# Performance work log

Hardware: AMD Instinct MI355X
Metric: run time of the kernel (lower is better)

The kernel has to match this reference:

```python
import jax, jax.numpy as jnp
import numpy as np

B, S = 2, 2048                 # batch, prefill seq len
H, HKV, D = 32, 8, 128          # num_heads, num_kv_heads, head_size
G = H // HKV                    # queries per kv head (GQA)
BLOCK_SIZE, NUM_BLOCKS = 128, 128
SCALE = 1.0 / (D ** 0.5)
NEG_INF = -1e9


def setup_inputs() -> dict:
    key = jax.random.key(0)
    kq, kk, kv, kc = jax.random.split(key, 4)
    query = jax.random.normal(kq, (B, S, H * D), dtype=jnp.float32)
    key_t = jax.random.normal(kk, (B, S, HKV * D), dtype=jnp.float32)
    value = jax.random.normal(kv, (B, S, HKV * D), dtype=jnp.float32)
    kv_cache = jax.random.normal(kc, (2, NUM_BLOCKS, BLOCK_SIZE, HKV, D), dtype=jnp.float32)
    tok = jnp.arange(B * S)
    block_indices = (tok // BLOCK_SIZE).astype(jnp.int32)   # in [0, NUM_BLOCKS)
    block_offsets = (tok % BLOCK_SIZE).astype(jnp.int32)    # in [0, BLOCK_SIZE)
    causal = jnp.tril(jnp.ones((S, S), dtype=bool))
    attn_bias = jnp.where(causal, 0.0, NEG_INF).astype(jnp.float32)[None, None]  # [1,1,S,S]
    return {"query": query, "key": key_t, "value": value, "kv_cache": kv_cache,
            "block_indices": block_indices, "block_offsets": block_offsets,
            "attn_bias": attn_bias}


def reference(query, key, value, kv_cache, block_indices, block_offsets, attn_bias):
    # --- KV cache scatter write (VLLMKVCache insert) ---
    k_tok = key.reshape(-1, HKV, D)     # [num_tokens, HKV, D]
    v_tok = value.reshape(-1, HKV, D)
    key_cache = kv_cache[0].at[block_indices, block_offsets].set(k_tok)
    value_cache = kv_cache[1].at[block_indices, block_offsets].set(v_tok)

    # --- prefill attention (xops.prompt_attention with GQA) ---
    q = query.reshape(B, S, HKV, G, D)            # split heads into kv groups
    kh = key.reshape(B, S, HKV, D)
    vh = value.reshape(B, S, HKV, D)
    scores = jnp.einsum('bqhgd,bkhd->bhgqk', q, kh) * SCALE  # [B,HKV,G,S,S]
    scores = scores + attn_bias[:, :, None]                   # bias broadcast over h,g
    probs = jax.nn.softmax(scores, axis=-1)
    out = jnp.einsum('bhgqk,bkhd->bqhgd', probs, vh)          # [B,S,HKV,G,D]
    output = out.reshape(B, S, H * D)
    return output, key_cache, value_cache
```

## Files before the change

kernel.cpp:

```cpp
#include <hip/hip_runtime.h>
#include <hip/hip_bf16.h>
#include <stdint.h>

#define B_ 2
#define S_ 2048
#define HKV_ 8
#define D_ 128

#define KVB 32
#define KTILE_SH 4096
#define VROWS 40
#define VTILE_SH 5120
#define LDSBUF 18432

typedef __attribute__((ext_vector_type(8))) short bf16x8;
typedef __attribute__((ext_vector_type(16))) float f32x16;
typedef __attribute__((ext_vector_type(4))) int int4v;

typedef const __attribute__((address_space(1))) void gv_t;
typedef __attribute__((address_space(3))) void lv_t;

__device__ __forceinline__ unsigned pk2(float lo, float hi) {
  unsigned r;
  asm("v_cvt_pk_bf16_f32 %0, %1, %2" : "=v"(r) : "v"(lo), "v"(hi));
  return r;
}
__device__ __forceinline__ void plswap(unsigned& a, unsigned& b) {
  asm volatile("v_permlane32_swap_b32 %0, %1" : "+v"(a), "+v"(b));
}
__device__ __forceinline__ bf16x8 frag4(unsigned a, unsigned b, unsigned c, unsigned d) {
  union { int4v i; bf16x8 v; } u;
  u.i = int4v{(int)a, (int)b, (int)c, (int)d};
  return u.v;
}


__global__ void cache_copy_kernel(const float4* __restrict__ src,
                                  float4* __restrict__ dst, int n4) {
  int i = blockIdx.x * blockDim.x + threadIdx.x;
  if (i < n4) dst[i] = src[i];
}


__global__ __launch_bounds__(256)
void prep_kernel(const float* __restrict__ K, const float* __restrict__ V,
                 const int* __restrict__ bi, const int* __restrict__ bo,
                 float* __restrict__ kc, float* __restrict__ vc,
                 short* __restrict__ kimg, short* __restrict__ vimg) {
  __shared__ float Vf[KVB * 132];
  const int bid = blockIdx.x;
  const int hg  = bid & 15;
  const int kt  = bid >> 4;
  const int kvh = hg & 7;
  const int b   = hg >> 3;
  const int tid = threadIdx.x;
  const int kv0 = kt * KVB;
  const float* kb = K + (int64_t)b * S_ * 1024 + kvh * 128;
  const float* vb = V + (int64_t)b * S_ * 1024 + kvh * 128;
  short* kimg_t = kimg + (int64_t)(hg * 64 + kt) * KTILE_SH;
  short* vimg_t = vimg + (int64_t)(hg * 64 + kt) * VTILE_SH;
#pragma unroll
  for (int i = 0; i < 4; ++i) {
    int idx = i * 256 + tid;
    int key = idx >> 5;
    int d0  = (idx & 31) * 4;
    int64_t roff = (int64_t)(kv0 + key) * 1024 + d0;
    float4 kf = *(const float4*)(kb + roff);
    float4 vf = *(const float4*)(vb + roff);
    int tok = b * S_ + kv0 + key;
    int64_t slot = (int64_t)bi[tok] * 128 + bo[tok];
    *(float4*)(kc + slot * 1024 + kvh * 128 + d0) = kf;
    *(float4*)(vc + slot * 1024 + kvh * 128 + d0) = vf;
    unsigned k01 = pk2(kf.x, kf.y), k23 = pk2(kf.z, kf.w);
    int koff = key * 128 + (d0 ^ ((key & 7) << 3));
    int2 st; st.x = (int)k01; st.y = (int)k23;
    *(int2*)(kimg_t + koff) = st;
    *(float4*)(&Vf[key * 132 + d0]) = vf;
  }
  __syncthreads();
  const int d  = tid & 127;
  const int kg = tid >> 7;
  const int k0 = kg * 16;
  unsigned uu[8];
#pragma unroll
  for (int i2 = 0; i2 < 8; ++i2)
    uu[i2] = pk2(Vf[(k0 + 2 * i2) * 132 + d], Vf[(k0 + 2 * i2 + 1) * 132 + d]);
  *(int4v*)(vimg_t + d * VROWS + k0)     = int4v{(int)uu[0], (int)uu[1], (int)uu[2], (int)uu[3]};
  *(int4v*)(vimg_t + d * VROWS + k0 + 8) = int4v{(int)uu[4], (int)uu[5], (int)uu[6], (int)uu[7]};
}


__global__ __launch_bounds__(256, 3)
void attn_kernel(const float* __restrict__ Q, const short* __restrict__ kimg,
                 const short* __restrict__ vimg, float* __restrict__ O) {
  __shared__ int4v ldsv[2 * LDSBUF / 16];
  char* ldsb = (char*)ldsv;

  const int bid = blockIdx.x;
  const int hg  = bid & 15;
  const int cc  = 63 - (bid >> 4);
  const int kvh = hg & 7;
  const int b   = hg >> 3;

  const int tid = threadIdx.x;
  const int w   = tid >> 6;
  const int l   = tid & 63;
  const int c31 = l & 31;
  const int hi  = l >> 5;
  const int qi  = c31 & 15;
  const int hh  = c31 >> 4;
  const int qoff = cc * 32 + (w & 1) * 16;
  const int qrow = qoff + qi;
  const int h    = kvh * 4 + (w >> 1) * 2 + hh;
  const int sw   = (c31 & 7) << 3;

  const float qscale = 0.08838834764831845f * 1.4426950408889634f;

  const float* qp = Q + ((int64_t)(b * S_ + qrow)) * 4096 + h * 128;
  bf16x8 qf[8];
#pragma unroll
  for (int ks = 0; ks < 8; ++ks) {
    int d0 = ks * 16 + hi * 8;
    float4 x = *(const float4*)(qp + d0);
    float4 y = *(const float4*)(qp + d0 + 4);
    qf[ks] = frag4(pk2(x.x * qscale, x.y * qscale), pk2(x.z * qscale, x.w * qscale),
                   pk2(y.x * qscale, y.y * qscale), pk2(y.z * qscale, y.w * qscale));
  }

  f32x16 acc[4];
#pragma unroll
  for (int dt = 0; dt < 4; ++dt)
#pragma unroll
    for (int r = 0; r < 16; ++r) acc[dt][r] = 0.f;
  float m = -1e30f, lsum = 0.f;

  const int nkt = cc + 1;
  const short* kimg_b = kimg + (int64_t)(hg * 64) * KTILE_SH;
  const short* vimg_b = vimg + (int64_t)(hg * 64) * VTILE_SH;

#define STAGE(KT, BUF)                                                          \
  do {                                                                          \
    const short* kg_ = kimg_b + (int64_t)(KT) * KTILE_SH;                       \
    const short* vg_ = vimg_b + (int64_t)(KT) * VTILE_SH;                       \
    char* kd_ = ldsb + (BUF) * LDSBUF;                                          \
    char* vd_ = kd_ + 8192;                                                     \
    _Pragma("unroll")                                                           \
    for (int i_ = 0; i_ < 2; ++i_) {                                            \
      int u_ = i_ * 256 + w * 64;                                               \
      __builtin_amdgcn_global_load_lds((gv_t*)(const void*)(kg_ + (u_ + l) * 8),\
                                       (lv_t*)(void*)(kd_ + u_ * 16), 16, 0, 0);\
    }                                                                           \
    _Pragma("unroll")                                                           \
    for (int i_ = 0; i_ < 3; ++i_) {                                            \
      int u_ = i_ * 256 + w * 64;                                               \
      if (u_ < 640) {                                                           \
        __builtin_amdgcn_global_load_lds((gv_t*)(const void*)(vg_ + (u_ + l) * 8),\
                                         (lv_t*)(void*)(vd_ + u_ * 16), 16, 0, 0);\
      }                                                                         \
    }                                                                           \
  } while (0)

  STAGE(0, 0);

  for (int kt = 0; kt < nkt; ++kt) {
    __syncthreads();
    const int cur = kt & 1;
    if (kt + 1 < nkt) STAGE(kt + 1, cur ^ 1);
    const short* kl = (const short*)(ldsb + cur * LDSBUF);
    const short* vl = (const short*)(ldsb + cur * LDSBUF + 8192);
    const int kv0 = kt * KVB;

    f32x16 s;
#pragma unroll
    for (int r = 0; r < 16; ++r) s[r] = 0.f;
#pragma unroll
    for (int ks = 0; ks < 8; ++ks) {
      int koff = c31 * 128 + ((ks * 16 + hi * 8) ^ sw);
      bf16x8 kf = *(const bf16x8*)(kl + koff);
      s = __builtin_amdgcn_mfma_f32_32x32x16_bf16(kf, qf[ks], s, 0, 0, 0);
    }

    if (kv0 + 31 > qoff) {
#pragma unroll
      for (int r = 0; r < 16; ++r) {
        int key = kv0 + (r & 3) + 8 * (r >> 2) + 4 * hi;
        if (key > qrow) s[r] = -1e30f;
      }
    }

    float qm = s[0];
#pragma unroll
    for (int r = 1; r < 16; ++r) qm = fmaxf(qm, s[r]);
    qm = fmaxf(qm, __shfl_xor(qm, 32));
    if (__any(qm > m + 11.0f)) {
      float mn = fmaxf(m, qm);
      float al = exp2f(m - mn);
      m = mn; lsum *= al;
#pragma unroll
      for (int dt = 0; dt < 4; ++dt)
#pragma unroll
        for (int r = 0; r < 16; ++r) acc[dt][r] *= al;
    }
    float su = 0.f;
#pragma unroll
    for (int r = 0; r < 16; ++r) {
      float p = exp2f(s[r] - m);
      s[r] = p;
      su += p;
    }
    lsum += su;

    unsigned u0 = pk2(s[0], s[1]),  u1 = pk2(s[2], s[3]);
    unsigned u2 = pk2(s[4], s[5]),  u3 = pk2(s[6], s[7]);
    unsigned u4 = pk2(s[8], s[9]),  u5 = pk2(s[10], s[11]);
    unsigned u6 = pk2(s[12], s[13]), u7 = pk2(s[14], s[15]);
    plswap(u0, u2); plswap(u1, u3);
    plswap(u4, u6); plswap(u5, u7);
    bf16x8 pf0 = frag4(u0, u1, u2, u3);
    bf16x8 pf1 = frag4(u4, u5, u6, u7);

#pragma unroll
    for (int ks2 = 0; ks2 < 2; ++ks2) {
      bf16x8 pf = ks2 ? pf1 : pf0;
#pragma unroll
      for (int dt = 0; dt < 4; ++dt) {
        const short* vp = vl + (dt * 32 + c31) * VROWS + ks2 * 16 + hi * 8;
        bf16x8 vf = *(const bf16x8*)vp;
        acc[dt] = __builtin_amdgcn_mfma_f32_32x32x16_bf16(vf, pf, acc[dt], 0, 0, 0);
      }
    }
  }
#undef STAGE

  float lt = lsum + __shfl_xor(lsum, 32);
  float inv = 1.0f / lt;
  __syncthreads();
  float* scr = (float*)ldsb + w * (32 * 33);
  float* ob = O + (int64_t)(b * S_) * 4096;
#pragma unroll
  for (int dt = 0; dt < 4; ++dt) {
#pragma unroll
    for (int r = 0; r < 16; ++r) {
      int crow = (r & 3) + 8 * (r >> 2) + 4 * hi;
      scr[c31 * 33 + crow] = acc[dt][r] * inv;
    }
    asm volatile("" ::: "memory");
#pragma unroll
    for (int rr = 0; rr < 16; ++rr) {
      int col = rr * 2 + hi;
      float val = scr[col * 33 + c31];
      int qi2 = col & 15, hh2 = col >> 4;
      int qq = cc * 32 + (w & 1) * 16 + qi2;
      int h2 = kvh * 4 + (w >> 1) * 2 + hh2;
      ob[(int64_t)qq * 4096 + h2 * 128 + dt * 32 + c31] = val;
    }
    asm volatile("" ::: "memory");
  }
}

extern "C" void kernel_launch(void* const* d_in, const int* in_sizes, int n_in,
                              void* d_out, int out_size, void* d_ws, size_t ws_size,
                              hipStream_t stream) {
  const float* Q   = (const float*)d_in[0];
  const float* K   = (const float*)d_in[1];
  const float* V   = (const float*)d_in[2];
  const float* kvc = (const float*)d_in[3];
  const int*   bi  = (const int*)d_in[4];
  const int*   bo  = (const int*)d_in[5];

  float* out = (float*)d_out;
  float* kc = out + (int64_t)B_ * S_ * 32 * 128;
  float* vc = kc + (int64_t)128 * 128 * HKV_ * D_;

  short* kimg = (short*)d_ws;
  short* vimg = kimg + (int64_t)1024 * KTILE_SH;

  const int n4 = (2 * 128 * 128 * HKV_ * D_) / 4;
  hipLaunchKernelGGL(cache_copy_kernel, dim3(n4 / 256), dim3(256), 0, stream,
                     (const float4*)kvc, (float4*)kc, n4);
  hipLaunchKernelGGL(prep_kernel, dim3(1024), dim3(256), 0, stream,
                     K, V, bi, bo, kc, vc, kimg, vimg);
  hipLaunchKernelGGL(attn_kernel, dim3(1024), dim3(256), 0, stream,
                     Q, kimg, vimg, out);
}
```

Before: 168.8 us.

## Fuse cache copy into attention launch, skip overwritten slots, relayout K/V tiles

Removes the separate full kv_cache copy kernel. Its work moves into extra blocks of the attention launch, which copy only the cache slots not written by the scatter, tracked through a per-slot byte map that is memset and then filled during prep. The K and V tile images are relaid out so each lane reads its MFMA fragment at a fixed stride without XOR swizzling. V tile padding is dropped and the launch bounds are raised to 4 blocks per CU. The change adds a memset launch and relies on the copy blocks and attention blocks sharing the GPU concurrently.

```diff
diff --git a/kernel.cpp b/kernel.cpp
--- a/kernel.cpp
+++ b/kernel.cpp
@@ -9,9 +9,11 @@
 
 #define KVB 32
 #define KTILE_SH 4096
-#define VROWS 40
-#define VTILE_SH 5120
-#define LDSBUF 18432
+#define VTILE_SH 4096
+#define LDSBUF 16384
+#define NCOPY 512
+#define PLANE4 4194304
+#define NSLOT 16384
 
 typedef __attribute__((ext_vector_type(8))) short bf16x8;
 typedef __attribute__((ext_vector_type(16))) float f32x16;
@@ -35,18 +37,12 @@
 }
 
 
-__global__ void cache_copy_kernel(const float4* __restrict__ src,
-                                  float4* __restrict__ dst, int n4) {
-  int i = blockIdx.x * blockDim.x + threadIdx.x;
-  if (i < n4) dst[i] = src[i];
-}
-
-
 __global__ __launch_bounds__(256)
 void prep_kernel(const float* __restrict__ K, const float* __restrict__ V,
                  const int* __restrict__ bi, const int* __restrict__ bo,
                  float* __restrict__ kc, float* __restrict__ vc,
-                 short* __restrict__ kimg, short* __restrict__ vimg) {
+                 short* __restrict__ kimg, short* __restrict__ vimg,
+                 unsigned char* __restrict__ map) {
   __shared__ float Vf[KVB * 132];
   const int bid = blockIdx.x;
   const int hg  = bid & 15;
@@ -68,11 +64,12 @@
     float4 kf = *(const float4*)(kb + roff);
     float4 vf = *(const float4*)(vb + roff);
     int tok = b * S_ + kv0 + key;
-    int64_t slot = (int64_t)bi[tok] * 128 + bo[tok];
-    *(float4*)(kc + slot * 1024 + kvh * 128 + d0) = kf;
-    *(float4*)(vc + slot * 1024 + kvh * 128 + d0) = vf;
+    int slot = bi[tok] * 128 + bo[tok];
+    *(float4*)(kc + (int64_t)slot * 1024 + kvh * 128 + d0) = kf;
+    *(float4*)(vc + (int64_t)slot * 1024 + kvh * 128 + d0) = vf;
+    if (d0 == 0 && kvh == 0) map[slot] = 1;
     unsigned k01 = pk2(kf.x, kf.y), k23 = pk2(kf.z, kf.w);
-    int koff = key * 128 + (d0 ^ ((key & 7) << 3));
+    int koff = (d0 >> 3) * 256 + key * 8 + (d0 & 7);
     int2 st; st.x = (int)k01; st.y = (int)k23;
     *(int2*)(kimg_t + koff) = st;
     *(float4*)(&Vf[key * 132 + d0]) = vf;
@@ -85,24 +82,38 @@
 #pragma unroll
   for (int i2 = 0; i2 < 8; ++i2)
     uu[i2] = pk2(Vf[(k0 + 2 * i2) * 132 + d], Vf[(k0 + 2 * i2 + 1) * 132 + d]);
-  *(int4v*)(vimg_t + d * VROWS + k0)     = int4v{(int)uu[0], (int)uu[1], (int)uu[2], (int)uu[3]};
-  *(int4v*)(vimg_t + d * VROWS + k0 + 8) = int4v{(int)uu[4], (int)uu[5], (int)uu[6], (int)uu[7]};
-}
-
-
-__global__ __launch_bounds__(256, 3)
-void attn_kernel(const float* __restrict__ Q, const short* __restrict__ kimg,
-                 const short* __restrict__ vimg, float* __restrict__ O) {
+  int vbase = ((d >> 5) * 4 + (k0 >> 4) * 2) * 256 + (d & 31) * 8;
+  *(int4v*)(vimg_t + vbase)       = int4v{(int)uu[0], (int)uu[1], (int)uu[2], (int)uu[3]};
+  *(int4v*)(vimg_t + vbase + 256) = int4v{(int)uu[4], (int)uu[5], (int)uu[6], (int)uu[7]};
+}
+
+
+__global__ __launch_bounds__(256, 4)
+void fused_kernel(const float* __restrict__ Q, const short* __restrict__ kimg,
+                  const short* __restrict__ vimg, const float4* __restrict__ kvc,
+                  float4* __restrict__ cdst, const unsigned char* __restrict__ map,
+                  float* __restrict__ O) {
   __shared__ int4v ldsv[2 * LDSBUF / 16];
   char* ldsb = (char*)ldsv;
 
   const int bid = blockIdx.x;
-  const int hg  = bid & 15;
-  const int cc  = 63 - (bid >> 4);
+  const int tid = threadIdx.x;
+
+  if (bid < NCOPY) {
+    const int n4 = 2 * PLANE4;
+    for (int idx = bid * 256 + tid; idx < n4; idx += NCOPY * 256) {
+      int f = idx & (PLANE4 - 1);
+      if (!map[f >> 8]) cdst[idx] = kvc[idx];
+    }
+    return;
+  }
+
+  const int abid = bid - NCOPY;
+  const int hg  = abid & 15;
+  const int cc  = 63 - (abid >> 4);
   const int kvh = hg & 7;
   const int b   = hg >> 3;
 
-  const int tid = threadIdx.x;
   const int w   = tid >> 6;
   const int l   = tid & 63;
   const int c31 = l & 31;
@@ -112,7 +123,6 @@
   const int qoff = cc * 32 + (w & 1) * 16;
   const int qrow = qoff + qi;
   const int h    = kvh * 4 + (w >> 1) * 2 + hh;
-  const int sw   = (c31 & 7) << 3;
 
   const float qscale = 0.08838834764831845f * 1.4426950408889634f;
 
@@ -138,26 +148,20 @@
   const short* kimg_b = kimg + (int64_t)(hg * 64) * KTILE_SH;
   const short* vimg_b = vimg + (int64_t)(hg * 64) * VTILE_SH;
 
-#define STAGE(KT, BUF)                                                          \
-  do {                                                                          \
-    const short* kg_ = kimg_b + (int64_t)(KT) * KTILE_SH;                       \
-    const short* vg_ = vimg_b + (int64_t)(KT) * VTILE_SH;                       \
-    char* kd_ = ldsb + (BUF) * LDSBUF;                                          \
-    char* vd_ = kd_ + 8192;                                                     \
-    _Pragma("unroll")                                                           \
-    for (int i_ = 0; i_ < 2; ++i_) {                                            \
-      int u_ = i_ * 256 + w * 64;                                               \
-      __builtin_amdgcn_global_load_lds((gv_t*)(const void*)(kg_ + (u_ + l) * 8),\
-                                       (lv_t*)(void*)(kd_ + u_ * 16), 16, 0, 0);\
-    }                                                                           \
-    _Pragma("unroll")                                                           \
-    for (int i_ = 0; i_ < 3; ++i_) {                                            \
-      int u_ = i_ * 256 + w * 64;                                               \
-      if (u_ < 640) {                                                           \
-        __builtin_amdgcn_global_load_lds((gv_t*)(const void*)(vg_ + (u_ + l) * 8),\
-                                         (lv_t*)(void*)(vd_ + u_ * 16), 16, 0, 0);\
-      }                                                                         \
-    }                                                                           \
+#define STAGE(KT, BUF)                                                           \
+  do {                                                                           \
+    const short* kg_ = kimg_b + (int64_t)(KT) * KTILE_SH;                        \
+    const short* vg_ = vimg_b + (int64_t)(KT) * VTILE_SH;                        \
+    char* kd_ = ldsb + (BUF) * LDSBUF;                                           \
+    char* vd_ = kd_ + 8192;                                                      \
+    _Pragma("unroll")                                                            \
+    for (int i_ = 0; i_ < 2; ++i_) {                                             \
+      int u_ = i_ * 256 + w * 64;                                                \
+      __builtin_amdgcn_global_load_lds((gv_t*)(const void*)(kg_ + (u_ + l) * 8), \
+                                       (lv_t*)(void*)(kd_ + u_ * 16), 16, 0, 0); \
+      __builtin_amdgcn_global_load_lds((gv_t*)(const void*)(vg_ + (u_ + l) * 8), \
+                                       (lv_t*)(void*)(vd_ + u_ * 16), 16, 0, 0); \
+    }                                                                            \
   } while (0)
 
   STAGE(0, 0);
@@ -166,8 +170,8 @@
     __syncthreads();
     const int cur = kt & 1;
     if (kt + 1 < nkt) STAGE(kt + 1, cur ^ 1);
-    const short* kl = (const short*)(ldsb + cur * LDSBUF);
-    const short* vl = (const short*)(ldsb + cur * LDSBUF + 8192);
+    const char* kfr = ldsb + cur * LDSBUF + hi * 512 + c31 * 16;
+    const char* vfr = kfr + 8192;
     const int kv0 = kt * KVB;
 
     f32x16 s;
@@ -175,8 +179,7 @@
     for (int r = 0; r < 16; ++r) s[r] = 0.f;
 #pragma unroll
     for (int ks = 0; ks < 8; ++ks) {
-      int koff = c31 * 128 + ((ks * 16 + hi * 8) ^ sw);
-      bf16x8 kf = *(const bf16x8*)(kl + koff);
+      bf16x8 kf = *(const bf16x8*)(kfr + ks * 1024);
       s = __builtin_amdgcn_mfma_f32_32x32x16_bf16(kf, qf[ks], s, 0, 0, 0);
     }
 
@@ -188,9 +191,14 @@
       }
     }
 
-    float qm = s[0];
-#pragma unroll
-    for (int r = 1; r < 16; ++r) qm = fmaxf(qm, s[r]);
+    float qm = fmaxf(fmaxf(s[0], s[1]), s[2]);
+    qm = fmaxf(fmaxf(qm, s[3]), s[4]);
+    qm = fmaxf(fmaxf(qm, s[5]), s[6]);
+    qm = fmaxf(fmaxf(qm, s[7]), s[8]);
+    qm = fmaxf(fmaxf(qm, s[9]), s[10]);
+    qm = fmaxf(fmaxf(qm, s[11]), s[12]);
+    qm = fmaxf(fmaxf(qm, s[13]), s[14]);
+    qm = fmaxf(qm, s[15]);
     qm = fmaxf(qm, __shfl_xor(qm, 32));
     if (__any(qm > m + 11.0f)) {
       float mn = fmaxf(m, qm);
@@ -210,9 +218,9 @@
     }
     lsum += su;
 
-    unsigned u0 = pk2(s[0], s[1]),  u1 = pk2(s[2], s[3]);
-    unsigned u2 = pk2(s[4], s[5]),  u3 = pk2(s[6], s[7]);
-    unsigned u4 = pk2(s[8], s[9]),  u5 = pk2(s[10], s[11]);
+    unsigned u0 = pk2(s[0], s[1]),   u1 = pk2(s[2], s[3]);
+    unsigned u2 = pk2(s[4], s[5]),   u3 = pk2(s[6], s[7]);
+    unsigned u4 = pk2(s[8], s[9]),   u5 = pk2(s[10], s[11]);
     unsigned u6 = pk2(s[12], s[13]), u7 = pk2(s[14], s[15]);
     plswap(u0, u2); plswap(u1, u3);
     plswap(u4, u6); plswap(u5, u7);
@@ -224,8 +232,7 @@
       bf16x8 pf = ks2 ? pf1 : pf0;
 #pragma unroll
       for (int dt = 0; dt < 4; ++dt) {
-        const short* vp = vl + (dt * 32 + c31) * VROWS + ks2 * 16 + hi * 8;
-        bf16x8 vf = *(const bf16x8*)vp;
+        bf16x8 vf = *(const bf16x8*)(vfr + (dt * 2 + ks2) * 1024);
         acc[dt] = __builtin_amdgcn_mfma_f32_32x32x16_bf16(vf, pf, acc[dt], 0, 0, 0);
       }
     }
@@ -274,12 +281,11 @@
 
   short* kimg = (short*)d_ws;
   short* vimg = kimg + (int64_t)1024 * KTILE_SH;
-
-  const int n4 = (2 * 128 * 128 * HKV_ * D_) / 4;
-  hipLaunchKernelGGL(cache_copy_kernel, dim3(n4 / 256), dim3(256), 0, stream,
-                     (const float4*)kvc, (float4*)kc, n4);
+  unsigned char* map = (unsigned char*)(vimg + (int64_t)1024 * VTILE_SH);
+
+  hipMemsetAsync(map, 0, NSLOT, stream);
   hipLaunchKernelGGL(prep_kernel, dim3(1024), dim3(256), 0, stream,
-                     K, V, bi, bo, kc, vc, kimg, vimg);
-  hipLaunchKernelGGL(attn_kernel, dim3(1024), dim3(256), 0, stream,
-                     Q, kimg, vimg, out);
-}
+                     K, V, bi, bo, kc, vc, kimg, vimg, map);
+  hipLaunchKernelGGL(fused_kernel, dim3(NCOPY + 1024), dim3(256), 0, stream,
+                     Q, kimg, vimg, (const float4*)kvc, (float4*)kc, map, out);
+}
```

Measured after the change: 194.8 us. 15.4% more time.
